# Kernel tuning notes

Measured on AMD Instinct MI355X. Metric: run time of the kernel, lower is better.

## Reference

```python
import jax, jax.numpy as jnp
import numpy as np

# Layer node counts: [n0, n1, n2, n3] for a 3-hop sampled subgraph
N_NODES = [524288, 65536, 8192, 1024]
DIMS = [100, 256, 256, 47]


def sage_conv(x_src, x_dst, src, dst, Wl, bl, Wr, n_dst):
    # PyG SAGEConv: lin_l(mean_agg(neighbors)) + lin_r(root)
    msg = x_src[src]                                        # [E, in]
    agg = jax.ops.segment_sum(msg, dst, num_segments=n_dst)  # [n_dst, in]
    cnt = jax.ops.segment_sum(jnp.ones((src.shape[0],), dtype=x_src.dtype), dst,
                              num_segments=n_dst)
    agg = agg / jnp.maximum(cnt, 1.0)[:, None]               # mean, 0-deg -> 0
    return agg @ Wl + bl + x_dst @ Wr


def setup_inputs() -> dict:
    key = jax.random.key(0)
    ks = jax.random.split(key, 20)
    inp = {"x": jax.random.normal(ks[0], (N_NODES[0], DIMS[0]), dtype=jnp.float32)}
    E = [655360, 81920, 10240]
    for i in range(3):
        inp[f"src{i}"] = jax.random.randint(ks[1 + 2 * i], (E[i],), 0, N_NODES[i])
        inp[f"dst{i}"] = jax.random.randint(ks[2 + 2 * i], (E[i],), 0, N_NODES[i + 1])
    for i in range(3):
        fin, fout = DIMS[i], DIMS[i + 1]
        inp[f"Wl{i}"] = jax.random.normal(ks[7 + 3 * i], (fin, fout), jnp.float32) * (1.0 / np.sqrt(fin))
        inp[f"bl{i}"] = jnp.zeros((fout,), jnp.float32)
        inp[f"Wr{i}"] = jax.random.normal(ks[8 + 3 * i], (fin, fout), jnp.float32) * (1.0 / np.sqrt(fin))
    return inp


def reference(x, src0, dst0, src1, dst1, src2, dst2,
              Wl0, bl0, Wr0, Wl1, bl1, Wr1, Wl2, bl2, Wr2):
    srcs = [src0, src1, src2]
    dsts = [dst0, dst1, dst2]
    Wls = [Wl0, Wl1, Wl2]
    bls = [bl0, bl1, bl2]
    Wrs = [Wr0, Wr1, Wr2]
    h = x
    for i in range(3):
        n_dst = N_NODES[i + 1]
        h_dst = h[:n_dst]
        h = sage_conv(h, h_dst, srcs[i], dsts[i], Wls[i], bls[i], Wrs[i], n_dst)
        if i != 2:
            h = jax.nn.relu(h)  # dropout is identity in eval mode
    return jax.nn.log_softmax(h, axis=-1)
```

## Files before the change

kernel.cpp:

```cpp
#include <hip/hip_runtime.h>
#include <math.h>

constexpr int NN1 = 65536, NN2 = 8192, NN3 = 1024;
constexpr int E0 = 655360, E1 = 81920, E2 = 10240;
constexpr int ETOT = E0 + E1 + E2;
constexpr int NTOT = NN1 + NN2 + NN3;

static inline int cdiv(int a, int b) { return (a + b - 1) / b; }

typedef __bf16 bf16x8_t __attribute__((ext_vector_type(8)));
typedef float f32x4_t __attribute__((ext_vector_type(4)));

__device__ __forceinline__ unsigned short f2bf(float f) {
    union { float f; unsigned int u; } v; v.f = f;
    unsigned int r = v.u + 0x7fffu + ((v.u >> 16) & 1u);
    return (unsigned short)(r >> 16);
}
__device__ __forceinline__ float bf2f(unsigned short h) {
    union { unsigned int u; float f; } v; v.u = ((unsigned int)h) << 16;
    return v.f;
}

constexpr int CB = (ETOT + 255) / 256;
__global__ void count_prep(const int* __restrict__ dst0, const int* __restrict__ dst1,
                           const int* __restrict__ dst2, int* __restrict__ cnt,
                           const float* __restrict__ Wl0, const float* __restrict__ Wr0,
                           unsigned short* __restrict__ Wt0a, unsigned short* __restrict__ Wt0b,
                           const float* __restrict__ Wl1, const float* __restrict__ Wr1,
                           unsigned short* __restrict__ Wt1a, unsigned short* __restrict__ Wt1b) {
    int b = blockIdx.x, t = threadIdx.x;
    if (b < CB) {
        int i = b * 256 + t;
        if (i < E0) atomicAdd(&cnt[dst0[i]], 1);
        else if (i < E0 + E1) atomicAdd(&cnt[NN1 + dst1[i - E0]], 1);
        else if (i < ETOT) atomicAdd(&cnt[NN1 + NN2 + dst2[i - E0 - E1]], 1);
        return;
    }
    b -= CB;
    if (b < 128) {
        int idx = b * 256 + t; int n = idx >> 7, k = idx & 127;
        Wt0a[idx] = f2bf(k < 100 ? Wl0[k * 256 + n] : 0.f);
    } else if (b < 256) {
        int idx = (b - 128) * 256 + t; int n = idx >> 7, k = idx & 127;
        Wt0b[idx] = f2bf(k < 100 ? Wr0[k * 256 + n] : 0.f);
    } else if (b < 512) {
        int idx = (b - 256) * 256 + t; int n = idx >> 8, k = idx & 255;
        Wt1a[idx] = f2bf(Wl1[k * 256 + n]);
    } else {
        int idx = (b - 512) * 256 + t; int n = idx >> 8, k = idx & 255;
        Wt1b[idx] = f2bf(Wr1[k * 256 + n]);
    }
}

__global__ __launch_bounds__(1024) void scan1(const int* __restrict__ cnt, int n,
                                              int* __restrict__ ofs, int* __restrict__ sums) {
    __shared__ int s[1024];
    int i = blockIdx.x * 1024 + threadIdx.x;
    int v = (i < n) ? cnt[i] : 0;
    s[threadIdx.x] = v;
    __syncthreads();
    for (int off = 1; off < 1024; off <<= 1) {
        int t = (threadIdx.x >= off) ? s[threadIdx.x - off] : 0;
        __syncthreads();
        s[threadIdx.x] += t;
        __syncthreads();
    }
    if (i < n) ofs[i] = s[threadIdx.x] - v;
    if (threadIdx.x == 1023) sums[blockIdx.x] = s[1023];
}

__global__ void scan3(const int* __restrict__ sums, int n,
                      int* __restrict__ ofs, int* __restrict__ cursor) {
    __shared__ int pref_s;
    int c = (blockIdx.x * 256) >> 10;
    if (threadIdx.x < 64) {
        int v = 0;
        for (int j = threadIdx.x; j < c; j += 64) v += sums[j];
        for (int o = 32; o; o >>= 1) v += __shfl_down(v, o);
        if (threadIdx.x == 0) pref_s = v;
    }
    __syncthreads();
    int i = blockIdx.x * 256 + threadIdx.x;
    if (i < n) {
        int v = ofs[i] + pref_s;
        ofs[i] = v;
        cursor[i] = v;
    }
    if (blockIdx.x == 0 && threadIdx.x == 0) ofs[n] = ETOT;
}

__global__ void scatter_all(const int* __restrict__ src0, const int* __restrict__ dst0,
                            const int* __restrict__ src1, const int* __restrict__ dst1,
                            const int* __restrict__ src2, const int* __restrict__ dst2,
                            int* __restrict__ cursor, int* __restrict__ perm) {
    int i = blockIdx.x * 256 + threadIdx.x;
    if (i < E0) {
        int p = atomicAdd(&cursor[dst0[i]], 1);
        perm[p] = src0[i];
    } else if (i < E0 + E1) {
        int j = i - E0;
        int p = atomicAdd(&cursor[NN1 + dst1[j]], 1);
        perm[p] = src1[j];
    } else if (i < ETOT) {
        int j = i - E0 - E1;
        int p = atomicAdd(&cursor[NN1 + NN2 + dst2[j]], 1);
        perm[p] = src2[j];
    }
}

__global__ __launch_bounds__(512, 4) void fused_l0(const float* __restrict__ x,
                                                   const int* __restrict__ perm,
                                                   const int* __restrict__ ofs,
                                                   const unsigned short* __restrict__ Wt0a,
                                                   const unsigned short* __restrict__ Wt0b,
                                                   const float* __restrict__ bias,
                                                   unsigned short* __restrict__ h1) {
    __shared__ unsigned short As[128][136];
    __shared__ unsigned short Bs[256][40];
    int tid = threadIdx.x;
    int lane = tid & 63, wid = tid >> 6;
    int bm = blockIdx.x * 128;

    {
        int g = lane >> 5, l5 = lane & 31;
        bool act = l5 < 25;
        int node0 = bm + wid * 16;
        int myofs = (lane < 17) ? ofs[node0 + lane] : 0;
        for (int r = 0; r < 16; ++r) {
            int row = wid * 16 + r;
            int s0 = __shfl(myofs, r), s1 = __shfl(myofs, r + 1);
            int deg = s1 - s0;
            float inv = 1.0f / fmaxf((float)deg, 1.0f);
            int dcap = min(deg, 64);
            int pe = (lane < dcap) ? perm[s0 + lane] : 0;
            f32x4_t A0 = {0.f, 0.f, 0.f, 0.f}, A1 = A0, A2 = A0, A3 = A0;
            for (int b = 0; b < dcap; b += 8) {
                int e0 = b + g, e1 = b + 2 + g, e2 = b + 4 + g, e3 = b + 6 + g;
                int p0 = __shfl(pe, e0), p1 = __shfl(pe, e1);
                int p2 = __shfl(pe, e2), p3 = __shfl(pe, e3);
                f32x4_t v0 = {0.f, 0.f, 0.f, 0.f}, v1 = v0, v2 = v0, v3 = v0;
                if (act && e0 < dcap) v0 = *reinterpret_cast<const f32x4_t*>(x + (size_t)p0 * 100 + l5 * 4);
                if (act && e1 < dcap) v1 = *reinterpret_cast<const f32x4_t*>(x + (size_t)p1 * 100 + l5 * 4);
                if (act && e2 < dcap) v2 = *reinterpret_cast<const f32x4_t*>(x + (size_t)p2 * 100 + l5 * 4);
                if (act && e3 < dcap) v3 = *reinterpret_cast<const f32x4_t*>(x + (size_t)p3 * 100 + l5 * 4);
                A0 += v0; A1 += v1; A2 += v2; A3 += v3;
            }
            for (int e = s0 + 64; e < s1; e += 2) {
                int idx = e + g;
                if (act && idx < s1)
                    A0 += *reinterpret_cast<const f32x4_t*>(x + (size_t)perm[idx] * 100 + l5 * 4);
            }
            f32x4_t a = (A0 + A1) + (A2 + A3);
#pragma unroll
            for (int c = 0; c < 4; c++) a[c] += __shfl_xor(a[c], 32);
            if (lane < 25) {
                ushort4 o;
                o.x = f2bf(a[0] * inv); o.y = f2bf(a[1] * inv);
                o.z = f2bf(a[2] * inv); o.w = f2bf(a[3] * inv);
                *reinterpret_cast<ushort4*>(&As[row][lane * 4]) = o;
            } else if (lane < 32) {
                *reinterpret_cast<ushort4*>(&As[row][100 + (lane - 25) * 4]) = make_ushort4(0, 0, 0, 0);
            }
        }
    }

    f32x4_t acc[4][4];
#pragma unroll
    for (int i = 0; i < 4; i++)
#pragma unroll
        for (int j = 0; j < 4; j++)
#pragma unroll
            for (int r = 0; r < 4; r++) acc[i][j][r] = 0.f;

    int r0 = lane & 15, kg = lane >> 4;
    int wm = (wid >> 2) * 64, wn = (wid & 3) * 64;

    for (int pass = 0; pass < 2; ++pass) {
        const unsigned short* W = pass ? Wt0b : Wt0a;
        if (pass) {
            __syncthreads();
            int rown = tid >> 2, q = tid & 3;
            for (int c4 = q; c4 < 25; c4 += 4) {
                f32x4_t v = *reinterpret_cast<const f32x4_t*>(x + (size_t)(bm + rown) * 100 + c4 * 4);
                ushort4 o;
                o.x = f2bf(v[0]); o.y = f2bf(v[1]); o.z = f2bf(v[2]); o.w = f2bf(v[3]);
                *reinterpret_cast<ushort4*>(&As[rown][c4 * 4]) = o;
            }
            if (q == 3) {
#pragma unroll
                for (int c4 = 25; c4 < 32; ++c4)
                    *reinterpret_cast<ushort4*>(&As[rown][c4 * 4]) = make_ushort4(0, 0, 0, 0);
            }
        }
        for (int ks = 0; ks < 4; ++ks) {
            __syncthreads();
            for (int c = tid; c < 1024; c += 512) {
                int n = c >> 2, k8 = (c & 3) << 3;
                *reinterpret_cast<int4*>(&Bs[n][k8]) =
                    *reinterpret_cast<const int4*>(&W[(size_t)n * 128 + ks * 32 + k8]);
            }
            __syncthreads();
            bf16x8_t af[4], bfv[4];
#pragma unroll
            for (int mi = 0; mi < 4; mi++)
                af[mi] = *reinterpret_cast<const bf16x8_t*>(&As[wm + mi * 16 + r0][ks * 32 + kg * 8]);
#pragma unroll
            for (int ni = 0; ni < 4; ni++)
                bfv[ni] = *reinterpret_cast<const bf16x8_t*>(&Bs[wn + ni * 16 + r0][kg * 8]);
#pragma unroll
            for (int mi = 0; mi < 4; mi++)
#pragma unroll
                for (int ni = 0; ni < 4; ni++)
                    acc[mi][ni] = __builtin_amdgcn_mfma_f32_16x16x32_bf16(af[mi], bfv[ni], acc[mi][ni], 0, 0, 0);
        }
    }

    int cc = lane & 15, rr = (lane >> 4) * 4;
#pragma unroll
    for (int mi = 0; mi < 4; mi++) {
#pragma unroll
        for (int ni = 0; ni < 4; ni++) {
            int col = wn + ni * 16 + cc;
            float b = bias[col];
#pragma unroll
            for (int j = 0; j < 4; j++) {
                int row = bm + wm + mi * 16 + rr + j;
                float v = fmaxf(acc[mi][ni][j] + b, 0.f);
                h1[(size_t)row * 256 + col] = f2bf(v);
            }
        }
    }
}

__global__ __launch_bounds__(512, 4) void fused_l1(const unsigned short* __restrict__ h1,
                                                   const int* __restrict__ perm,
                                                   const int* __restrict__ ofs,
                                                   const unsigned short* __restrict__ Wt1a,
                                                   const unsigned short* __restrict__ Wt1b,
                                                   const float* __restrict__ bias,
                                                   float* __restrict__ h2) {
    __shared__ unsigned short As[64][264];
    __shared__ unsigned short Bs[128][40];
    int tid = threadIdx.x;
    int lane = tid & 63, wid = tid >> 6;
    int bm = blockIdx.y * 64, bn = blockIdx.x * 128;

    {
        int node0 = bm + wid * 8;
        int myofs = (lane < 9) ? ofs[node0 + lane] : 0;
        for (int r = 0; r < 8; ++r) {
            int row = wid * 8 + r;
            int s0 = __shfl(myofs, r), s1 = __shfl(myofs, r + 1);
            int deg = s1 - s0;
            float inv = 1.0f / fmaxf((float)deg, 1.0f);
            int dcap = min(deg, 64);
            int pe = (lane < dcap) ? perm[s0 + lane] : 0;
            float ac[4][4] = {};
            for (int b = 0; b < dcap; b += 4) {
#pragma unroll
                for (int u = 0; u < 4; u++) {
                    int pu = __shfl(pe, b + u);
                    ushort4 v = make_ushort4(0, 0, 0, 0);
                    if (b + u < dcap)
                        v = *reinterpret_cast<const ushort4*>(h1 + (size_t)pu * 256 + lane * 4);
                    ac[u][0] += bf2f(v.x); ac[u][1] += bf2f(v.y);
                    ac[u][2] += bf2f(v.z); ac[u][3] += bf2f(v.w);
                }
            }
            for (int e = s0 + 64; e < s1; e++) {
                ushort4 v = *reinterpret_cast<const ushort4*>(h1 + (size_t)perm[e] * 256 + lane * 4);
                ac[0][0] += bf2f(v.x); ac[0][1] += bf2f(v.y);
                ac[0][2] += bf2f(v.z); ac[0][3] += bf2f(v.w);
            }
            ushort4 o;
            o.x = f2bf((ac[0][0] + ac[1][0] + ac[2][0] + ac[3][0]) * inv);
            o.y = f2bf((ac[0][1] + ac[1][1] + ac[2][1] + ac[3][1]) * inv);
            o.z = f2bf((ac[0][2] + ac[1][2] + ac[2][2] + ac[3][2]) * inv);
            o.w = f2bf((ac[0][3] + ac[1][3] + ac[2][3] + ac[3][3]) * inv);
            *reinterpret_cast<ushort4*>(&As[row][lane * 4]) = o;
        }
    }

    f32x4_t acc[2][2];
#pragma unroll
    for (int i = 0; i < 2; i++)
#pragma unroll
        for (int j = 0; j < 2; j++)
#pragma unroll
            for (int r = 0; r < 4; r++) acc[i][j][r] = 0.f;

    int r0 = lane & 15, kg = lane >> 4;
    int wm = (wid >> 2) * 32, wn = (wid & 3) * 32;

    for (int pass = 0; pass < 2; ++pass) {
        const unsigned short* W = pass ? Wt1b : Wt1a;
        if (pass) {
            __syncthreads();
            for (int c = tid; c < 2048; c += 512) {
                int row = c >> 5, k8 = (c & 31) << 3;
                *reinterpret_cast<int4*>(&As[row][k8]) =
                    *reinterpret_cast<const int4*>(&h1[(size_t)(bm + row) * 256 + k8]);
            }
        }
        for (int ks = 0; ks < 8; ++ks) {
            __syncthreads();
            {
                int c = tid;
                int n = c >> 2, k8 = (c & 3) << 3;
                *reinterpret_cast<int4*>(&Bs[n][k8]) =
                    *reinterpret_cast<const int4*>(&W[(size_t)(bn + n) * 256 + ks * 32 + k8]);
            }
            __syncthreads();
            bf16x8_t af[2], bfv[2];
#pragma unroll
            for (int mi = 0; mi < 2; mi++)
                af[mi] = *reinterpret_cast<const bf16x8_t*>(&As[wm + mi * 16 + r0][ks * 32 + kg * 8]);
#pragma unroll
            for (int ni = 0; ni < 2; ni++)
                bfv[ni] = *reinterpret_cast<const bf16x8_t*>(&Bs[wn + ni * 16 + r0][kg * 8]);
#pragma unroll
            for (int mi = 0; mi < 2; mi++)
#pragma unroll
                for (int ni = 0; ni < 2; ni++)
                    acc[mi][ni] = __builtin_amdgcn_mfma_f32_16x16x32_bf16(af[mi], bfv[ni], acc[mi][ni], 0, 0, 0);
        }
    }

    int cc = lane & 15, rr = (lane >> 4) * 4;
#pragma unroll
    for (int mi = 0; mi < 2; mi++) {
#pragma unroll
        for (int ni = 0; ni < 2; ni++) {
            int col = bn + wn + ni * 16 + cc;
            float b = bias[col];
#pragma unroll
            for (int j = 0; j < 4; j++) {
                int row = bm + wm + mi * 16 + rr + j;
                h2[(size_t)row * 256 + col] = fmaxf(acc[mi][ni][j] + b, 0.f);
            }
        }
    }
}

__global__ __launch_bounds__(256) void gemm2_all(const float* __restrict__ h2,
                                                 const int* __restrict__ perm,
                                                 const int* __restrict__ ofs,
                                                 const float* __restrict__ W1,
                                                 const float* __restrict__ W2,
                                                 const float* __restrict__ bias,
                                                 float* __restrict__ out,
                                                 int M, int N) {
    __shared__ float Agg[64][260];
    __shared__ float As[16][65];
    __shared__ float Bs[16][64];
    int tid = threadIdx.x;
    int lane = tid & 63, wid = tid >> 6;
    int bm = blockIdx.y * 64;

    {
        int node0 = bm + wid * 16;
        int myofs = (lane < 17) ? ofs[node0 + lane] : 0;
        for (int r = 0; r < 16; ++r) {
            int row = wid * 16 + r;
            int s0 = __shfl(myofs, r), s1 = __shfl(myofs, r + 1);
            int deg = s1 - s0;
            float inv = 1.0f / fmaxf((float)deg, 1.0f);
            int dcap = min(deg, 64);
            int pe = (lane < dcap) ? perm[s0 + lane] : 0;
            f32x4_t B0 = {0.f, 0.f, 0.f, 0.f}, B1 = B0, B2 = B0, B3 = B0;
            for (int b = 0; b < dcap; b += 4) {
                int p0 = __shfl(pe, b), p1 = __shfl(pe, b + 1);
                int p2 = __shfl(pe, b + 2), p3 = __shfl(pe, b + 3);
                f32x4_t v0 = {0.f, 0.f, 0.f, 0.f}, v1 = v0, v2 = v0, v3 = v0;
                if (b < dcap)     v0 = *reinterpret_cast<const f32x4_t*>(h2 + (size_t)p0 * 256 + lane * 4);
                if (b + 1 < dcap) v1 = *reinterpret_cast<const f32x4_t*>(h2 + (size_t)p1 * 256 + lane * 4);
                if (b + 2 < dcap) v2 = *reinterpret_cast<const f32x4_t*>(h2 + (size_t)p2 * 256 + lane * 4);
                if (b + 3 < dcap) v3 = *reinterpret_cast<const f32x4_t*>(h2 + (size_t)p3 * 256 + lane * 4);
                B0 += v0; B1 += v1; B2 += v2; B3 += v3;
            }
            for (int e = s0 + 64; e < s1; e++)
                B0 += *reinterpret_cast<const f32x4_t*>(h2 + (size_t)perm[e] * 256 + lane * 4);
            f32x4_t a = (B0 + B1) + (B2 + B3);
#pragma unroll
            for (int c = 0; c < 4; c++) Agg[row][lane * 4 + c] = a[c] * inv;
        }
    }
    __syncthreads();

    int tx = tid & 15, ty = tid >> 4;
    float acc[4][4] = {};
    for (int pass = 0; pass < 2; ++pass) {
        const float* W = pass ? W2 : W1;
        for (int k0 = 0; k0 < 256; k0 += 16) {
            __syncthreads();
#pragma unroll
            for (int i = 0; i < 4; i++) {
                int L = i * 256 + tid;
                int m = L >> 4, k = L & 15;
                As[k][m] = pass ? h2[(size_t)(bm + m) * 256 + k0 + k] : Agg[m][k0 + k];
            }
#pragma unroll
            for (int i = 0; i < 4; i++) {
                int L = i * 256 + tid;
                int n = L & 63, k = L >> 6;
                float v = 0.f;
                if (n < N) v = W[(size_t)(k0 + k) * N + n];
                Bs[k][n] = v;
            }
            __syncthreads();
#pragma unroll
            for (int k = 0; k < 16; k++) {
                float a[4], b[4];
#pragma unroll
                for (int i = 0; i < 4; i++) a[i] = As[k][ty * 4 + i];
#pragma unroll
                for (int j = 0; j < 4; j++) b[j] = Bs[k][tx * 4 + j];
#pragma unroll
                for (int i = 0; i < 4; i++)
#pragma unroll
                    for (int j = 0; j < 4; j++) acc[i][j] += a[i] * b[j];
            }
        }
    }
#pragma unroll
    for (int i = 0; i < 4; i++) {
        int gm = bm + ty * 4 + i;
        float vals[4];
        float vmax = -1e30f;
#pragma unroll
        for (int j = 0; j < 4; j++) {
            int gn = tx * 4 + j;
            vals[j] = (gn < N) ? acc[i][j] + bias[gn] : -1e30f;
            vmax = fmaxf(vmax, vals[j]);
        }
#pragma unroll
        for (int o = 1; o < 16; o <<= 1) vmax = fmaxf(vmax, __shfl_xor(vmax, o));
        float se = 0.f;
#pragma unroll
        for (int j = 0; j < 4; j++) {
            int gn = tx * 4 + j;
            if (gn < N) se += expf(vals[j] - vmax);
        }
#pragma unroll
        for (int o = 1; o < 16; o <<= 1) se += __shfl_xor(se, o);
        float ls = logf(se);
#pragma unroll
        for (int j = 0; j < 4; j++) {
            int gn = tx * 4 + j;
            if (gn < N && gm < M) out[(size_t)gm * N + gn] = vals[j] - vmax - ls;
        }
    }
}

extern "C" void kernel_launch(void* const* d_in, const int* in_sizes, int n_in,
                              void* d_out, int out_size, void* d_ws, size_t ws_size,
                              hipStream_t stream) {
    const float* x   = (const float*)d_in[0];
    const int* src0  = (const int*)d_in[1];
    const int* dst0  = (const int*)d_in[2];
    const int* src1  = (const int*)d_in[3];
    const int* dst1  = (const int*)d_in[4];
    const int* src2  = (const int*)d_in[5];
    const int* dst2  = (const int*)d_in[6];
    const float* Wl0 = (const float*)d_in[7];
    const float* bl0 = (const float*)d_in[8];
    const float* Wr0 = (const float*)d_in[9];
    const float* Wl1 = (const float*)d_in[10];
    const float* bl1 = (const float*)d_in[11];
    const float* Wr1 = (const float*)d_in[12];
    const float* Wl2 = (const float*)d_in[13];
    const float* bl2 = (const float*)d_in[14];
    const float* Wr2 = (const float*)d_in[15];
    float* out = (float*)d_out;

    char* p = (char*)d_ws;
    auto alloc = [&](size_t bytes) { char* r = p; p += (bytes + 255) & ~(size_t)255; return r; };
    unsigned short* h1   = (unsigned short*)alloc((size_t)NN1 * 256 * 2);
    float* h2    = (float*)alloc((size_t)NN2 * 256 * 4);
    unsigned short* Wt0a = (unsigned short*)alloc(256 * 128 * 2);
    unsigned short* Wt0b = (unsigned short*)alloc(256 * 128 * 2);
    unsigned short* Wt1a = (unsigned short*)alloc(256 * 256 * 2);
    unsigned short* Wt1b = (unsigned short*)alloc(256 * 256 * 2);
    int* cnt    = (int*)alloc((size_t)NTOT * 4);
    int* ofs    = (int*)alloc((size_t)(NTOT + 1) * 4);
    int* cursor = (int*)alloc((size_t)(NTOT + 1) * 4);
    int* sums   = (int*)alloc(128 * 4);
    int* perm   = (int*)alloc((size_t)ETOT * 4);

    hipMemsetAsync(cnt, 0, (size_t)NTOT * 4, stream);
    count_prep<<<CB + 768, 256, 0, stream>>>(dst0, dst1, dst2, cnt,
                                             Wl0, Wr0, Wt0a, Wt0b, Wl1, Wr1, Wt1a, Wt1b);
    int nb = cdiv(NTOT, 1024);
    scan1<<<nb, 1024, 0, stream>>>(cnt, NTOT, ofs, sums);
    scan3<<<cdiv(NTOT, 256), 256, 0, stream>>>(sums, NTOT, ofs, cursor);
    scatter_all<<<cdiv(ETOT, 256), 256, 0, stream>>>(src0, dst0, src1, dst1, src2, dst2, cursor, perm);

    fused_l0<<<NN1 / 128, 512, 0, stream>>>(x, perm, ofs, Wt0a, Wt0b, bl0, h1);

    {
        dim3 grid(2, NN2 / 64);
        fused_l1<<<grid, 512, 0, stream>>>(h1, perm, ofs + NN1, Wt1a, Wt1b, bl1, h2);
    }

    {
        dim3 grid(1, NN3 / 64);
        gemm2_all<<<grid, 256, 0, stream>>>(h2, perm, ofs + NN1 + NN2, Wl2, Wr2, bl2, out, NN3, 47);
    }
}
```

Measured before the change: 272.9 us.

## Read GEMM weights directly from global, widen l1 tiles, split layer-2 aggregation

In fused_l0 and fused_l1 the weight tiles are no longer staged through shared memory. MFMA B fragments are loaded directly from global/L2, which drops two barriers per k-step. fused_l1 now has each block cover all 256 output columns with a 64-row tile, so the neighbour gather is no longer duplicated across two column blocks. Layer 2 splits into a separate wave-per-row mean aggregation kernel and a generic fp32 GEMM, adding a launch and an intermediate buffer. The launch_bounds occupancy hint is removed.

```diff
diff --git a/kernel.cpp b/kernel.cpp
--- a/kernel.cpp
+++ b/kernel.cpp
@@ -108,15 +108,14 @@
     }
 }
 
-__global__ __launch_bounds__(512, 4) void fused_l0(const float* __restrict__ x,
-                                                   const int* __restrict__ perm,
-                                                   const int* __restrict__ ofs,
-                                                   const unsigned short* __restrict__ Wt0a,
-                                                   const unsigned short* __restrict__ Wt0b,
-                                                   const float* __restrict__ bias,
-                                                   unsigned short* __restrict__ h1) {
+__global__ __launch_bounds__(512) void fused_l0(const float* __restrict__ x,
+                                                const int* __restrict__ perm,
+                                                const int* __restrict__ ofs,
+                                                const unsigned short* __restrict__ Wt0a,
+                                                const unsigned short* __restrict__ Wt0b,
+                                                const float* __restrict__ bias,
+                                                unsigned short* __restrict__ h1) {
     __shared__ unsigned short As[128][136];
-    __shared__ unsigned short Bs[256][40];
     int tid = threadIdx.x;
     int lane = tid & 63, wid = tid >> 6;
     int bm = blockIdx.x * 128;
@@ -192,21 +191,16 @@
                     *reinterpret_cast<ushort4*>(&As[rown][c4 * 4]) = make_ushort4(0, 0, 0, 0);
             }
         }
+        __syncthreads();
+#pragma unroll
         for (int ks = 0; ks < 4; ++ks) {
-            __syncthreads();
-            for (int c = tid; c < 1024; c += 512) {
-                int n = c >> 2, k8 = (c & 3) << 3;
-                *reinterpret_cast<int4*>(&Bs[n][k8]) =
-                    *reinterpret_cast<const int4*>(&W[(size_t)n * 128 + ks * 32 + k8]);
-            }
-            __syncthreads();
             bf16x8_t af[4], bfv[4];
+#pragma unroll
+            for (int ni = 0; ni < 4; ni++)
+                bfv[ni] = *reinterpret_cast<const bf16x8_t*>(&W[(size_t)(wn + ni * 16 + r0) * 128 + ks * 32 + kg * 8]);
 #pragma unroll
             for (int mi = 0; mi < 4; mi++)
                 af[mi] = *reinterpret_cast<const bf16x8_t*>(&As[wm + mi * 16 + r0][ks * 32 + kg * 8]);
-#pragma unroll
-            for (int ni = 0; ni < 4; ni++)
-                bfv[ni] = *reinterpret_cast<const bf16x8_t*>(&Bs[wn + ni * 16 + r0][kg * 8]);
 #pragma unroll
             for (int mi = 0; mi < 4; mi++)
 #pragma unroll
@@ -232,18 +226,17 @@
     }
 }
 
-__global__ __launch_bounds__(512, 4) void fused_l1(const unsigned short* __restrict__ h1,
-                                                   const int* __restrict__ perm,
-                                                   const int* __restrict__ ofs,
-                                                   const unsigned short* __restrict__ Wt1a,
-                                                   const unsigned short* __restrict__ Wt1b,
-                                                   const float* __restrict__ bias,
-                                                   float* __restrict__ h2) {
+__global__ __launch_bounds__(512) void fused_l1(const unsigned short* __restrict__ h1,
+                                                const int* __restrict__ perm,
+                                                const int* __restrict__ ofs,
+                                                const unsigned short* __restrict__ Wt1a,
+                                                const unsigned short* __restrict__ Wt1b,
+                                                const float* __restrict__ bias,
+                                                float* __restrict__ h2) {
     __shared__ unsigned short As[64][264];
-    __shared__ unsigned short Bs[128][40];
     int tid = threadIdx.x;
     int lane = tid & 63, wid = tid >> 6;
-    int bm = blockIdx.y * 64, bn = blockIdx.x * 128;
+    int bm = blockIdx.x * 64;
 
     {
         int node0 = bm + wid * 8;
@@ -281,16 +274,16 @@
         }
     }
 
-    f32x4_t acc[2][2];
-#pragma unroll
-    for (int i = 0; i < 2; i++)
+    f32x4_t acc[4][2];
+#pragma unroll
+    for (int i = 0; i < 4; i++)
 #pragma unroll
         for (int j = 0; j < 2; j++)
 #pragma unroll
             for (int r = 0; r < 4; r++) acc[i][j][r] = 0.f;
 
     int r0 = lane & 15, kg = lane >> 4;
-    int wm = (wid >> 2) * 32, wn = (wid & 3) * 32;
+    int wn = wid * 32;
 
     for (int pass = 0; pass < 2; ++pass) {
         const unsigned short* W = pass ? Wt1b : Wt1a;
@@ -302,24 +295,18 @@
                     *reinterpret_cast<const int4*>(&h1[(size_t)(bm + row) * 256 + k8]);
             }
         }
+        __syncthreads();
+#pragma unroll
         for (int ks = 0; ks < 8; ++ks) {
-            __syncthreads();
-            {
-                int c = tid;
-                int n = c >> 2, k8 = (c & 3) << 3;
-                *reinterpret_cast<int4*>(&Bs[n][k8]) =
-                    *reinterpret_cast<const int4*>(&W[(size_t)(bn + n) * 256 + ks * 32 + k8]);
-            }
-            __syncthreads();
-            bf16x8_t af[2], bfv[2];
-#pragma unroll
-            for (int mi = 0; mi < 2; mi++)
-                af[mi] = *reinterpret_cast<const bf16x8_t*>(&As[wm + mi * 16 + r0][ks * 32 + kg * 8]);
+            bf16x8_t af[4], bfv[2];
 #pragma unroll
             for (int ni = 0; ni < 2; ni++)
-                bfv[ni] = *reinterpret_cast<const bf16x8_t*>(&Bs[wn + ni * 16 + r0][kg * 8]);
-#pragma unroll
-            for (int mi = 0; mi < 2; mi++)
+                bfv[ni] = *reinterpret_cast<const bf16x8_t*>(&W[(size_t)(wn + ni * 16 + r0) * 256 + ks * 32 + kg * 8]);
+#pragma unroll
+            for (int mi = 0; mi < 4; mi++)
+                af[mi] = *reinterpret_cast<const bf16x8_t*>(&As[mi * 16 + r0][ks * 32 + kg * 8]);
+#pragma unroll
+            for (int mi = 0; mi < 4; mi++)
 #pragma unroll
                 for (int ni = 0; ni < 2; ni++)
                     acc[mi][ni] = __builtin_amdgcn_mfma_f32_16x16x32_bf16(af[mi], bfv[ni], acc[mi][ni], 0, 0, 0);
@@ -328,83 +315,68 @@
 
     int cc = lane & 15, rr = (lane >> 4) * 4;
 #pragma unroll
-    for (int mi = 0; mi < 2; mi++) {
+    for (int mi = 0; mi < 4; mi++) {
 #pragma unroll
         for (int ni = 0; ni < 2; ni++) {
-            int col = bn + wn + ni * 16 + cc;
+            int col = wn + ni * 16 + cc;
             float b = bias[col];
 #pragma unroll
             for (int j = 0; j < 4; j++) {
-                int row = bm + wm + mi * 16 + rr + j;
+                int row = bm + mi * 16 + rr + j;
                 h2[(size_t)row * 256 + col] = fmaxf(acc[mi][ni][j] + b, 0.f);
             }
         }
     }
 }
 
-__global__ __launch_bounds__(256) void gemm2_all(const float* __restrict__ h2,
-                                                 const int* __restrict__ perm,
-                                                 const int* __restrict__ ofs,
-                                                 const float* __restrict__ W1,
-                                                 const float* __restrict__ W2,
-                                                 const float* __restrict__ bias,
-                                                 float* __restrict__ out,
-                                                 int M, int N) {
-    __shared__ float Agg[64][260];
+__global__ void agg_vec4_256(const float* __restrict__ x, const int* __restrict__ perm,
+                             const int* __restrict__ ofs, float* __restrict__ agg, int nrows) {
+    int wave = (blockIdx.x * blockDim.x + threadIdx.x) >> 6;
+    int lane = threadIdx.x & 63;
+    if (wave >= nrows) return;
+    int s0 = ofs[wave], s1 = ofs[wave + 1];
+    float4 acc = make_float4(0.f, 0.f, 0.f, 0.f);
+    for (int e = s0; e < s1; e++) {
+        const float4* xr = (const float4*)(x + (size_t)perm[e] * 256);
+        float4 v = xr[lane];
+        acc.x += v.x; acc.y += v.y; acc.z += v.z; acc.w += v.w;
+    }
+    float inv = 1.0f / fmaxf((float)(s1 - s0), 1.0f);
+    acc.x *= inv; acc.y *= inv; acc.z *= inv; acc.w *= inv;
+    ((float4*)(agg + (size_t)wave * 256))[lane] = acc;
+}
+
+__global__ __launch_bounds__(256) void gemm2_fused(const float* __restrict__ A1, const float* __restrict__ W1, int K1,
+                                                   const float* __restrict__ A2, const float* __restrict__ W2, int K2,
+                                                   const float* __restrict__ bias, float* __restrict__ out,
+                                                   int M, int N) {
     __shared__ float As[16][65];
     __shared__ float Bs[16][64];
     int tid = threadIdx.x;
-    int lane = tid & 63, wid = tid >> 6;
+    int tx = tid & 15, ty = tid >> 4;
     int bm = blockIdx.y * 64;
-
-    {
-        int node0 = bm + wid * 16;
-        int myofs = (lane < 17) ? ofs[node0 + lane] : 0;
-        for (int r = 0; r < 16; ++r) {
-            int row = wid * 16 + r;
-            int s0 = __shfl(myofs, r), s1 = __shfl(myofs, r + 1);
-            int deg = s1 - s0;
-            float inv = 1.0f / fmaxf((float)deg, 1.0f);
-            int dcap = min(deg, 64);
-            int pe = (lane < dcap) ? perm[s0 + lane] : 0;
-            f32x4_t B0 = {0.f, 0.f, 0.f, 0.f}, B1 = B0, B2 = B0, B3 = B0;
-            for (int b = 0; b < dcap; b += 4) {
-                int p0 = __shfl(pe, b), p1 = __shfl(pe, b + 1);
-                int p2 = __shfl(pe, b + 2), p3 = __shfl(pe, b + 3);
-                f32x4_t v0 = {0.f, 0.f, 0.f, 0.f}, v1 = v0, v2 = v0, v3 = v0;
-                if (b < dcap)     v0 = *reinterpret_cast<const f32x4_t*>(h2 + (size_t)p0 * 256 + lane * 4);
-                if (b + 1 < dcap) v1 = *reinterpret_cast<const f32x4_t*>(h2 + (size_t)p1 * 256 + lane * 4);
-                if (b + 2 < dcap) v2 = *reinterpret_cast<const f32x4_t*>(h2 + (size_t)p2 * 256 + lane * 4);
-                if (b + 3 < dcap) v3 = *reinterpret_cast<const f32x4_t*>(h2 + (size_t)p3 * 256 + lane * 4);
-                B0 += v0; B1 += v1; B2 += v2; B3 += v3;
-            }
-            for (int e = s0 + 64; e < s1; e++)
-                B0 += *reinterpret_cast<const f32x4_t*>(h2 + (size_t)perm[e] * 256 + lane * 4);
-            f32x4_t a = (B0 + B1) + (B2 + B3);
-#pragma unroll
-            for (int c = 0; c < 4; c++) Agg[row][lane * 4 + c] = a[c] * inv;
-        }
-    }
-    __syncthreads();
-
-    int tx = tid & 15, ty = tid >> 4;
     float acc[4][4] = {};
     for (int pass = 0; pass < 2; ++pass) {
+        const float* A = pass ? A2 : A1;
         const float* W = pass ? W2 : W1;
-        for (int k0 = 0; k0 < 256; k0 += 16) {
-            __syncthreads();
+        int K = pass ? K2 : K1;
+        for (int k0 = 0; k0 < K; k0 += 16) {
 #pragma unroll
             for (int i = 0; i < 4; i++) {
                 int L = i * 256 + tid;
                 int m = L >> 4, k = L & 15;
-                As[k][m] = pass ? h2[(size_t)(bm + m) * 256 + k0 + k] : Agg[m][k0 + k];
+                int gm = bm + m, gk = k0 + k;
+                float v = 0.f;
+                if (gm < M && gk < K) v = A[(size_t)gm * K + gk];
+                As[k][m] = v;
             }
 #pragma unroll
             for (int i = 0; i < 4; i++) {
                 int L = i * 256 + tid;
                 int n = L & 63, k = L >> 6;
+                int gk = k0 + k;
                 float v = 0.f;
-                if (n < N) v = W[(size_t)(k0 + k) * N + n];
+                if (gk < K && n < N) v = W[(size_t)gk * N + n];
                 Bs[k][n] = v;
             }
             __syncthreads();
@@ -420,6 +392,7 @@
 #pragma unroll
                     for (int j = 0; j < 4; j++) acc[i][j] += a[i] * b[j];
             }
+            __syncthreads();
         }
     }
 #pragma unroll
@@ -477,6 +450,7 @@
     auto alloc = [&](size_t bytes) { char* r = p; p += (bytes + 255) & ~(size_t)255; return r; };
     unsigned short* h1   = (unsigned short*)alloc((size_t)NN1 * 256 * 2);
     float* h2    = (float*)alloc((size_t)NN2 * 256 * 4);
+    float* agg2  = (float*)alloc((size_t)NN3 * 256 * 4);
     unsigned short* Wt0a = (unsigned short*)alloc(256 * 128 * 2);
     unsigned short* Wt0b = (unsigned short*)alloc(256 * 128 * 2);
     unsigned short* Wt1a = (unsigned short*)alloc(256 * 256 * 2);
@@ -497,13 +471,11 @@
 
     fused_l0<<<NN1 / 128, 512, 0, stream>>>(x, perm, ofs, Wt0a, Wt0b, bl0, h1);
 
-    {
-        dim3 grid(2, NN2 / 64);
-        fused_l1<<<grid, 512, 0, stream>>>(h1, perm, ofs + NN1, Wt1a, Wt1b, bl1, h2);
-    }
-
+    fused_l1<<<NN2 / 64, 512, 0, stream>>>(h1, perm, ofs + NN1, Wt1a, Wt1b, bl1, h2);
+
+    agg_vec4_256<<<cdiv(NN3 * 64, 256), 256, 0, stream>>>(h2, perm, ofs + NN1 + NN2, agg2, NN3);
     {
         dim3 grid(1, NN3 / 64);
-        gemm2_all<<<grid, 256, 0, stream>>>(h2, perm, ofs + NN1 + NN2, Wl2, Wr2, bl2, out, NN3, 47);
-    }
-}
+        gemm2_fused<<<grid, 256, 0, stream>>>(agg2, Wl2, 256, h2, Wr2, 256, bl2, out, NN3, 47);
+    }
+}
```

After: 302.1 us. 1.11x slower.

## Shrink layer-0 tile to 64 rows, gather two nodes per iteration with prefetch

Applied to the files above, without the earlier changes.

The layer-0 fused kernel now handles 64 destination rows per block instead of 128, doubling the grid, and each wave computes a 64x32 output slice instead of 64x64. The gather loop processes two destination nodes at a time with twice as many independent loads in flight, and prefetches the next pair's offsets and neighbour indices. The launch-bounds occupancy hint is dropped from both fused kernels. The aim is more memory-level parallelism and better load balance in the bandwidth-bound gather. The cost is that the weight tile is reloaded from global memory twice as often across blocks and register pressure goes up.

```diff
diff --git a/kernel.cpp b/kernel.cpp
--- a/kernel.cpp
+++ b/kernel.cpp
@@ -108,90 +108,134 @@
     }
 }
 
-__global__ __launch_bounds__(512, 4) void fused_l0(const float* __restrict__ x,
-                                                   const int* __restrict__ perm,
-                                                   const int* __restrict__ ofs,
-                                                   const unsigned short* __restrict__ Wt0a,
-                                                   const unsigned short* __restrict__ Wt0b,
-                                                   const float* __restrict__ bias,
-                                                   unsigned short* __restrict__ h1) {
-    __shared__ unsigned short As[128][136];
+__global__ __launch_bounds__(512) void fused_l0(const float* __restrict__ x,
+                                                const int* __restrict__ perm,
+                                                const int* __restrict__ ofs,
+                                                const unsigned short* __restrict__ Wt0a,
+                                                const unsigned short* __restrict__ Wt0b,
+                                                const float* __restrict__ bias,
+                                                unsigned short* __restrict__ h1) {
+    __shared__ unsigned short As[64][136];
     __shared__ unsigned short Bs[256][40];
     int tid = threadIdx.x;
     int lane = tid & 63, wid = tid >> 6;
-    int bm = blockIdx.x * 128;
+    int bm = blockIdx.x * 64;
 
     {
         int g = lane >> 5, l5 = lane & 31;
         bool act = l5 < 25;
-        int node0 = bm + wid * 16;
-        int myofs = (lane < 17) ? ofs[node0 + lane] : 0;
-        for (int r = 0; r < 16; ++r) {
-            int row = wid * 16 + r;
-            int s0 = __shfl(myofs, r), s1 = __shfl(myofs, r + 1);
-            int deg = s1 - s0;
-            float inv = 1.0f / fmaxf((float)deg, 1.0f);
-            int dcap = min(deg, 64);
-            int pe = (lane < dcap) ? perm[s0 + lane] : 0;
+        int node0 = bm + wid * 8;
+        int myofs = (lane < 9) ? ofs[node0 + lane] : 0;
+
+        int s0a = __shfl(myofs, 0);
+        int s0b = __shfl(myofs, 1);
+        int s1b = __shfl(myofs, 2);
+        int dega = s0b - s0a, degb = s1b - s0b;
+        int dca = min(dega, 64), dcb = min(degb, 64);
+        int pea = (lane < dca) ? perm[s0a + lane] : 0;
+        int peb = (lane < dcb) ? perm[s0b + lane] : 0;
+
+        for (int r = 0; r < 8; r += 2) {
+            int s0a_n = 0, s0b_n = 0, dega_n = 0, degb_n = 0, dca_n = 0, dcb_n = 0;
+            int pea_n = 0, peb_n = 0;
+            if (r + 2 < 8) {
+                s0a_n = __shfl(myofs, r + 2);
+                s0b_n = __shfl(myofs, r + 3);
+                int s1b_n = __shfl(myofs, r + 4);
+                dega_n = s0b_n - s0a_n; degb_n = s1b_n - s0b_n;
+                dca_n = min(dega_n, 64); dcb_n = min(degb_n, 64);
+                pea_n = (lane < dca_n) ? perm[s0a_n + lane] : 0;
+                peb_n = (lane < dcb_n) ? perm[s0b_n + lane] : 0;
+            }
             f32x4_t A0 = {0.f, 0.f, 0.f, 0.f}, A1 = A0, A2 = A0, A3 = A0;
-            for (int b = 0; b < dcap; b += 8) {
+            f32x4_t B0 = A0, B1 = A0, B2 = A0, B3 = A0;
+            int mx = max(dca, dcb);
+            for (int b = 0; b < mx; b += 8) {
                 int e0 = b + g, e1 = b + 2 + g, e2 = b + 4 + g, e3 = b + 6 + g;
-                int p0 = __shfl(pe, e0), p1 = __shfl(pe, e1);
-                int p2 = __shfl(pe, e2), p3 = __shfl(pe, e3);
-                f32x4_t v0 = {0.f, 0.f, 0.f, 0.f}, v1 = v0, v2 = v0, v3 = v0;
-                if (act && e0 < dcap) v0 = *reinterpret_cast<const f32x4_t*>(x + (size_t)p0 * 100 + l5 * 4);
-                if (act && e1 < dcap) v1 = *reinterpret_cast<const f32x4_t*>(x + (size_t)p1 * 100 + l5 * 4);
-                if (act && e2 < dcap) v2 = *reinterpret_cast<const f32x4_t*>(x + (size_t)p2 * 100 + l5 * 4);
-                if (act && e3 < dcap) v3 = *reinterpret_cast<const f32x4_t*>(x + (size_t)p3 * 100 + l5 * 4);
-                A0 += v0; A1 += v1; A2 += v2; A3 += v3;
-            }
-            for (int e = s0 + 64; e < s1; e += 2) {
+                int pa0 = __shfl(pea, e0), pa1 = __shfl(pea, e1);
+                int pa2 = __shfl(pea, e2), pa3 = __shfl(pea, e3);
+                int pb0 = __shfl(peb, e0), pb1 = __shfl(peb, e1);
+                int pb2 = __shfl(peb, e2), pb3 = __shfl(peb, e3);
+                f32x4_t z = {0.f, 0.f, 0.f, 0.f};
+                f32x4_t va0 = z, va1 = z, va2 = z, va3 = z;
+                f32x4_t vb0 = z, vb1 = z, vb2 = z, vb3 = z;
+                if (act && e0 < dca) va0 = *reinterpret_cast<const f32x4_t*>(x + (size_t)pa0 * 100 + l5 * 4);
+                if (act && e1 < dca) va1 = *reinterpret_cast<const f32x4_t*>(x + (size_t)pa1 * 100 + l5 * 4);
+                if (act && e2 < dca) va2 = *reinterpret_cast<const f32x4_t*>(x + (size_t)pa2 * 100 + l5 * 4);
+                if (act && e3 < dca) va3 = *reinterpret_cast<const f32x4_t*>(x + (size_t)pa3 * 100 + l5 * 4);
+                if (act && e0 < dcb) vb0 = *reinterpret_cast<const f32x4_t*>(x + (size_t)pb0 * 100 + l5 * 4);
+                if (act && e1 < dcb) vb1 = *reinterpret_cast<const f32x4_t*>(x + (size_t)pb1 * 100 + l5 * 4);
+                if (act && e2 < dcb) vb2 = *reinterpret_cast<const f32x4_t*>(x + (size_t)pb2 * 100 + l5 * 4);
+                if (act && e3 < dcb) vb3 = *reinterpret_cast<const f32x4_t*>(x + (size_t)pb3 * 100 + l5 * 4);
+                A0 += va0; A1 += va1; A2 += va2; A3 += va3;
+                B0 += vb0; B1 += vb1; B2 += vb2; B3 += vb3;
+            }
+            for (int e = s0a + 64; e < s0a + dega; e += 2) {
                 int idx = e + g;
-                if (act && idx < s1)
+                if (act && idx < s0a + dega)
                     A0 += *reinterpret_cast<const f32x4_t*>(x + (size_t)perm[idx] * 100 + l5 * 4);
             }
+            for (int e = s0b + 64; e < s0b + degb; e += 2) {
+                int idx = e + g;
+                if (act && idx < s0b + degb)
+                    B0 += *reinterpret_cast<const f32x4_t*>(x + (size_t)perm[idx] * 100 + l5 * 4);
+            }
             f32x4_t a = (A0 + A1) + (A2 + A3);
-#pragma unroll
-            for (int c = 0; c < 4; c++) a[c] += __shfl_xor(a[c], 32);
+            f32x4_t bb = (B0 + B1) + (B2 + B3);
+#pragma unroll
+            for (int c = 0; c < 4; c++) {
+                a[c] += __shfl_xor(a[c], 32);
+                bb[c] += __shfl_xor(bb[c], 32);
+            }
+            float inva = 1.0f / fmaxf((float)dega, 1.0f);
+            float invb = 1.0f / fmaxf((float)degb, 1.0f);
+            int rowa = wid * 8 + r, rowb = rowa + 1;
             if (lane < 25) {
-                ushort4 o;
-                o.x = f2bf(a[0] * inv); o.y = f2bf(a[1] * inv);
-                o.z = f2bf(a[2] * inv); o.w = f2bf(a[3] * inv);
-                *reinterpret_cast<ushort4*>(&As[row][lane * 4]) = o;
+                ushort4 oa, ob;
+                oa.x = f2bf(a[0] * inva); oa.y = f2bf(a[1] * inva);
+                oa.z = f2bf(a[2] * inva); oa.w = f2bf(a[3] * inva);
+                ob.x = f2bf(bb[0] * invb); ob.y = f2bf(bb[1] * invb);
+                ob.z = f2bf(bb[2] * invb); ob.w = f2bf(bb[3] * invb);
+                *reinterpret_cast<ushort4*>(&As[rowa][lane * 4]) = oa;
+                *reinterpret_cast<ushort4*>(&As[rowb][lane * 4]) = ob;
             } else if (lane < 32) {
-                *reinterpret_cast<ushort4*>(&As[row][100 + (lane - 25) * 4]) = make_ushort4(0, 0, 0, 0);
-            }
-        }
-    }
-
-    f32x4_t acc[4][4];
+                ushort4 z4 = make_ushort4(0, 0, 0, 0);
+                *reinterpret_cast<ushort4*>(&As[rowa][100 + (lane - 25) * 4]) = z4;
+                *reinterpret_cast<ushort4*>(&As[rowb][100 + (lane - 25) * 4]) = z4;
+            }
+            s0a = s0a_n; s0b = s0b_n; dega = dega_n; degb = degb_n;
+            dca = dca_n; dcb = dcb_n; pea = pea_n; peb = peb_n;
+        }
+    }
+
+    f32x4_t acc[4][2];
 #pragma unroll
     for (int i = 0; i < 4; i++)
 #pragma unroll
-        for (int j = 0; j < 4; j++)
+        for (int j = 0; j < 2; j++)
 #pragma unroll
             for (int r = 0; r < 4; r++) acc[i][j][r] = 0.f;
 
     int r0 = lane & 15, kg = lane >> 4;
-    int wm = (wid >> 2) * 64, wn = (wid & 3) * 64;
+    int wn = wid * 32;
 
     for (int pass = 0; pass < 2; ++pass) {
         const unsigned short* W = pass ? Wt0b : Wt0a;
         if (pass) {
             __syncthreads();
-            int rown = tid >> 2, q = tid & 3;
-            for (int c4 = q; c4 < 25; c4 += 4) {
-                f32x4_t v = *reinterpret_cast<const f32x4_t*>(x + (size_t)(bm + rown) * 100 + c4 * 4);
-                ushort4 o;
-                o.x = f2bf(v[0]); o.y = f2bf(v[1]); o.z = f2bf(v[2]); o.w = f2bf(v[3]);
-                *reinterpret_cast<ushort4*>(&As[rown][c4 * 4]) = o;
-            }
-            if (q == 3) {
-#pragma unroll
-                for (int c4 = 25; c4 < 32; ++c4)
-                    *reinterpret_cast<ushort4*>(&As[rown][c4 * 4]) = make_ushort4(0, 0, 0, 0);
-            }
-        }
+            for (int c = tid; c < 2048; c += 512) {
+                int row = c >> 5, c4 = c & 31;
+                if (c4 < 25) {
+                    f32x4_t v = *reinterpret_cast<const f32x4_t*>(x + (size_t)(bm + row) * 100 + c4 * 4);
+                    ushort4 o;
+                    o.x = f2bf(v[0]); o.y = f2bf(v[1]); o.z = f2bf(v[2]); o.w = f2bf(v[3]);
+                    *reinterpret_cast<ushort4*>(&As[row][c4 * 4]) = o;
+                } else {
+                    *reinterpret_cast<ushort4*>(&As[row][c4 * 4]) = make_ushort4(0, 0, 0, 0);
+                }
+            }
+        }
+#pragma unroll
         for (int ks = 0; ks < 4; ++ks) {
             __syncthreads();
             for (int c = tid; c < 1024; c += 512) {
@@ -200,17 +244,17 @@
                     *reinterpret_cast<const int4*>(&W[(size_t)n * 128 + ks * 32 + k8]);
             }
             __syncthreads();
-            bf16x8_t af[4], bfv[4];
+            bf16x8_t af[4], bfv[2];
+#pragma unroll
+            for (int ni = 0; ni < 2; ni++)
+                bfv[ni] = *reinterpret_cast<const bf16x8_t*>(&Bs[wn + ni * 16 + r0][kg * 8]);
 #pragma unroll
             for (int mi = 0; mi < 4; mi++)
-                af[mi] = *reinterpret_cast<const bf16x8_t*>(&As[wm + mi * 16 + r0][ks * 32 + kg * 8]);
-#pragma unroll
-            for (int ni = 0; ni < 4; ni++)
-                bfv[ni] = *reinterpret_cast<const bf16x8_t*>(&Bs[wn + ni * 16 + r0][kg * 8]);
+                af[mi] = *reinterpret_cast<const bf16x8_t*>(&As[mi * 16 + r0][ks * 32 + kg * 8]);
 #pragma unroll
             for (int mi = 0; mi < 4; mi++)
 #pragma unroll
-                for (int ni = 0; ni < 4; ni++)
+                for (int ni = 0; ni < 2; ni++)
                     acc[mi][ni] = __builtin_amdgcn_mfma_f32_16x16x32_bf16(af[mi], bfv[ni], acc[mi][ni], 0, 0, 0);
         }
     }
@@ -219,12 +263,12 @@
 #pragma unroll
     for (int mi = 0; mi < 4; mi++) {
 #pragma unroll
-        for (int ni = 0; ni < 4; ni++) {
+        for (int ni = 0; ni < 2; ni++) {
             int col = wn + ni * 16 + cc;
             float b = bias[col];
 #pragma unroll
             for (int j = 0; j < 4; j++) {
-                int row = bm + wm + mi * 16 + rr + j;
+                int row = bm + mi * 16 + rr + j;
                 float v = fmaxf(acc[mi][ni][j] + b, 0.f);
                 h1[(size_t)row * 256 + col] = f2bf(v);
             }
@@ -232,13 +276,13 @@
     }
 }
 
-__global__ __launch_bounds__(512, 4) void fused_l1(const unsigned short* __restrict__ h1,
-                                                   const int* __restrict__ perm,
-                                                   const int* __restrict__ ofs,
-                                                   const unsigned short* __restrict__ Wt1a,
-                                                   const unsigned short* __restrict__ Wt1b,
-                                                   const float* __restrict__ bias,
-                                                   float* __restrict__ h2) {
+__global__ __launch_bounds__(512) void fused_l1(const unsigned short* __restrict__ h1,
+                                                const int* __restrict__ perm,
+                                                const int* __restrict__ ofs,
+                                                const unsigned short* __restrict__ Wt1a,
+                                                const unsigned short* __restrict__ Wt1b,
+                                                const float* __restrict__ bias,
+                                                float* __restrict__ h2) {
     __shared__ unsigned short As[64][264];
     __shared__ unsigned short Bs[128][40];
     int tid = threadIdx.x;
@@ -495,7 +539,7 @@
     scan3<<<cdiv(NTOT, 256), 256, 0, stream>>>(sums, NTOT, ofs, cursor);
     scatter_all<<<cdiv(ETOT, 256), 256, 0, stream>>>(src0, dst0, src1, dst1, src2, dst2, cursor, perm);
 
-    fused_l0<<<NN1 / 128, 512, 0, stream>>>(x, perm, ofs, Wt0a, Wt0b, bl0, h1);
+    fused_l0<<<NN1 / 64, 512, 0, stream>>>(x, perm, ofs, Wt0a, Wt0b, bl0, h1);
 
     {
         dim3 grid(2, NN2 / 64);
```

Measured after the change: 276.6 us. Within noise of the previous version (+1.4%).
